# Kernel tuning notes

Hardware: AMD Instinct MI355X
Metric: run time of the kernel (lower is better)

## Reference

```python
import jax, jax.numpy as jnp
import numpy as np

B, S, D = 2, 2048, 2048
H, KV, HD = 32, 8, 64
REP = H // KV  # 4


def setup_inputs() -> dict:
    key = jax.random.key(0)
    ks = jax.random.split(key, 5)
    x = jax.random.normal(ks[0], (B, S, D), jnp.float32)
    # Llama rope frequencies: theta=10000, pairs of adjacent dims
    inv_freq = 1.0 / (10000.0 ** (np.arange(0, HD, 2, dtype=np.float64) / HD))  # [HD/2]
    ang = np.outer(np.arange(S, dtype=np.float64), inv_freq)  # [S, HD/2]
    freqs_cis = jnp.asarray(np.stack([np.cos(ang), np.sin(ang)], axis=-1), jnp.float32)  # [S, HD/2, 2]
    wq = jax.random.normal(ks[1], (H * HD, D), jnp.float32) * 0.02
    wk = jax.random.normal(ks[2], (KV * HD, D), jnp.float32) * 0.02
    wv = jax.random.normal(ks[3], (KV * HD, D), jnp.float32) * 0.02
    wo = jax.random.normal(ks[4], (D, H * HD), jnp.float32) * 0.02
    return {"x": x, "freqs_cis": freqs_cis, "wq": wq, "wk": wk, "wv": wv, "wo": wo}


def _apply_rope(t, cos, sin):
    # t: [B,S,nh,HD]; cos/sin: [S,HD/2]; complex multiply on adjacent pairs
    b, s, nh, hd = t.shape
    t2 = t.reshape(b, s, nh, hd // 2, 2)
    tr, ti = t2[..., 0], t2[..., 1]
    c = cos[None, :, None, :]
    sn = sin[None, :, None, :]
    out = jnp.stack([tr * c - ti * sn, tr * sn + ti * c], axis=-1)
    return out.reshape(b, s, nh, hd)


def reference(x, freqs_cis, wq, wk, wv, wo):
    # QKV projections (torch Linear: y = x @ W.T)
    q = jnp.einsum('bsd,ed->bse', x, wq).reshape(B, S, H, HD)
    k = jnp.einsum('bsd,ed->bse', x, wk).reshape(B, S, KV, HD)
    v = jnp.einsum('bsd,ed->bse', x, wv).reshape(B, S, KV, HD)
    cos, sin = freqs_cis[..., 0], freqs_cis[..., 1]
    q = _apply_rope(q, cos, sin)
    k = _apply_rope(k, cos, sin)
    # GQA without materializing repeated K/V: group query heads by KV head
    qg = q.reshape(B, S, KV, REP, HD)
    scale = 1.0 / jnp.sqrt(jnp.asarray(HD, q.dtype))
    scores = jnp.einsum('bsgrd,btgd->bgrst', qg, k) * scale  # [B,KV,REP,S,S]
    causal = jnp.tril(jnp.ones((S, S), bool))
    scores = jnp.where(causal, scores, -jnp.inf)
    p = jax.nn.softmax(scores, axis=-1)
    o = jnp.einsum('bgrst,btgd->bsgrd', p, v).reshape(B, S, H * HD)
    return jnp.einsum('bse,de->bsd', o, wo)
```

## Files before the change

kernel.cpp:

```cpp
#include <hip/hip_runtime.h>
#include <cstdint>
#include <cstddef>

#define B_ 2
#define S_ 2048
#define D_ 2048
#define H_ 32
#define KV_ 8
#define HD_ 64
#define M_ (B_*S_)
#define EQ_ (H_*HD_)
#define EK_ (KV_*HD_)

typedef unsigned short u16;
typedef __attribute__((ext_vector_type(8))) short s16x8;
typedef __attribute__((ext_vector_type(4))) float f32x4;

#define QSCALE 0.18033688011112042f
#define EXPOFF 15.869645449778564f

#if __has_builtin(__builtin_amdgcn_exp2f)
#define EXP2(x) __builtin_amdgcn_exp2f(x)
#else
#define EXP2(x) __expf((x) * 0.6931471805599453f)
#endif

__device__ __forceinline__ u16 f2bf(float f) {
  unsigned u = __float_as_uint(f);
  u += 0x7fffu + ((u >> 16) & 1u);
  return (u16)(u >> 16);
}
__device__ __forceinline__ unsigned pk2(float a, float b) {
  unsigned ua = __float_as_uint(a) + 0x8000u;
  unsigned ub = __float_as_uint(b) + 0x8000u;
  return __builtin_amdgcn_perm(ub, ua, 0x07060302);
}
__device__ __forceinline__ f32x4 mfma16(s16x8 a, s16x8 b, f32x4 c) {
  return __builtin_amdgcn_mfma_f32_16x16x32_bf16(a, b, c, 0, 0, 0);
}
__device__ __forceinline__ void gl_lds16(const void* g, void* l) {
  __builtin_amdgcn_global_load_lds(
      (const __attribute__((address_space(1))) void*)g,
      (__attribute__((address_space(3))) void*)l, 16, 0, 0);
}

__global__ void cast_all(const float4* __restrict__ x, const float4* __restrict__ wq,
                         const float4* __restrict__ wk, const float4* __restrict__ wv,
                         const float4* __restrict__ wo, ushort4* __restrict__ dst) {
  int i = blockIdx.x * 256 + threadIdx.x;
  const float4* src; int off;
  if (i < 2097152)      { src = x;  off = i; }
  else if (i < 3145728) { src = wq; off = i - 2097152; }
  else if (i < 3407872) { src = wk; off = i - 3145728; }
  else if (i < 3670016) { src = wv; off = i - 3407872; }
  else                  { src = wo; off = i - 3670016; }
  float4 v = src[off];
  ushort4 r;
  r.x = f2bf(v.x); r.y = f2bf(v.y); r.z = f2bf(v.z); r.w = f2bf(v.w);
  dst[i] = r;
}

__global__ __launch_bounds__(256)
void gemm_qkv(const u16* __restrict__ A, const u16* __restrict__ Bw,
              u16* __restrict__ qb, u16* __restrict__ kb, u16* __restrict__ vtb,
              const float* __restrict__ fc) {
  __shared__ __align__(16) u16 As[128 * 64];
  __shared__ __align__(16) u16 Bs[96 * 64];
  const int tid  = threadIdx.x;
  const int lane = tid & 63;
  const int wave = tid >> 6;
  const int m0 = blockIdx.y * 128;
  const int n0 = blockIdx.x * 96;
  const int wm = (wave >> 1) * 64;
  const int wn = (wave & 1) * 48;
  const int l15 = lane & 15;
  const int quad = lane >> 4;

  f32x4 acc[4][3] = {};

  for (int k0 = 0; k0 < D_; k0 += 64) {
    #pragma unroll
    for (int rr = 0; rr < 4; ++rr) {
      int c = tid + rr * 256;
      int row = c >> 3;
      int ksrc = ((c & 7) ^ (row & 7)) * 8;
      gl_lds16(A + (size_t)(m0 + row) * D_ + k0 + ksrc, &As[c * 8]);
    }
    #pragma unroll
    for (int rr = 0; rr < 3; ++rr) {
      int c = tid + rr * 256;
      int row = c >> 3;
      int ksrc = ((c & 7) ^ (row & 7)) * 8;
      gl_lds16(Bw + (size_t)(n0 + row) * D_ + k0 + ksrc, &Bs[c * 8]);
    }
    __syncthreads();

    #pragma unroll
    for (int kc = 0; kc < 2; ++kc) {
      s16x8 af[4], bfr[3];
      #pragma unroll
      for (int mi = 0; mi < 4; ++mi) {
        int row = wm + mi * 16 + l15;
        af[mi]  = *(const s16x8*)&As[row * 64 + (((kc * 4 + quad) ^ (row & 7)) * 8)];
      }
      #pragma unroll
      for (int ni = 0; ni < 3; ++ni) {
        int row = wn + ni * 16 + l15;
        bfr[ni] = *(const s16x8*)&Bs[row * 64 + (((kc * 4 + quad) ^ (row & 7)) * 8)];
      }
      #pragma unroll
      for (int mi = 0; mi < 4; ++mi)
        #pragma unroll
        for (int ni = 0; ni < 3; ++ni)
          acc[mi][ni] = mfma16(af[mi], bfr[ni], acc[mi][ni]);
    }
    __syncthreads();
  }

  const float sg = (l15 & 1) ? 1.f : -1.f;
  #pragma unroll
  for (int mi = 0; mi < 4; ++mi) {
    #pragma unroll
    for (int ni = 0; ni < 3; ++ni) {
      const int col = n0 + wn + ni * 16 + l15;
      if (col < 2560) {
        const bool isQ = (col < 2048);
        u16* dst = isQ ? qb : kb;
        const int ncol0 = isQ ? 0 : 2048;
        const int ndim  = isQ ? EQ_ : EK_;
        const float scale = isQ ? QSCALE : 1.0f;
        const int ip = (col & 63) >> 1;
        #pragma unroll
        for (int r = 0; r < 4; ++r) {
          int row = m0 + wm + mi * 16 + quad * 4 + r;
          const float* fr = fc + (size_t)(row & (S_ - 1)) * 64;
          float c  = fr[ip * 2];
          float sn = fr[ip * 2 + 1];
          float v = acc[mi][ni][r];
          float p = __shfl_xor(v, 1, 64);
          float o = (v * c + sg * (p * sn)) * scale;
          dst[(size_t)row * ndim + col - ncol0] = f2bf(o);
        }
      } else {
        const int vcol = col - 2560;
        uint2 w;
        w.x = pk2(acc[mi][ni][0], acc[mi][ni][1]);
        w.y = pk2(acc[mi][ni][2], acc[mi][ni][3]);
        *(uint2*)(vtb + (size_t)vcol * M_ + m0 + wm + mi * 16 + quad * 4) = w;
      }
    }
  }
}

__global__ __launch_bounds__(256)
void gemm_o(const u16* __restrict__ A, const u16* __restrict__ Bw, float* __restrict__ C,
            int Ndim, int Kdim) {
  __shared__ __align__(16) u16 As[64 * 64];
  __shared__ __align__(16) u16 Bs[128 * 64];
  const int tid  = threadIdx.x;
  const int lane = tid & 63;
  const int wave = tid >> 6;
  const int m0 = blockIdx.y * 64;
  const int n0 = blockIdx.x * 128;
  const int wm = (wave >> 1) * 32;
  const int wn = (wave & 1) * 64;
  const int l15 = lane & 15;
  const int quad = lane >> 4;

  f32x4 acc[2][4] = {};

  for (int k0 = 0; k0 < Kdim; k0 += 64) {
    #pragma unroll
    for (int rr = 0; rr < 2; ++rr) {
      int c = tid + rr * 256;
      int row = c >> 3;
      int ksrc = ((c & 7) ^ (row & 7)) * 8;
      gl_lds16(A + (size_t)(m0 + row) * Kdim + k0 + ksrc, &As[c * 8]);
    }
    #pragma unroll
    for (int rr = 0; rr < 4; ++rr) {
      int c = tid + rr * 256;
      int row = c >> 3;
      int ksrc = ((c & 7) ^ (row & 7)) * 8;
      gl_lds16(Bw + (size_t)(n0 + row) * Kdim + k0 + ksrc, &Bs[c * 8]);
    }
    __syncthreads();

    #pragma unroll
    for (int kc = 0; kc < 2; ++kc) {
      s16x8 af[2], bfr[4];
      #pragma unroll
      for (int mi = 0; mi < 2; ++mi) {
        int row = wm + mi * 16 + l15;
        af[mi]  = *(const s16x8*)&As[row * 64 + (((kc * 4 + quad) ^ (row & 7)) * 8)];
      }
      #pragma unroll
      for (int ni = 0; ni < 4; ++ni) {
        int row = wn + ni * 16 + l15;
        bfr[ni] = *(const s16x8*)&Bs[row * 64 + (((kc * 4 + quad) ^ (row & 7)) * 8)];
      }
      #pragma unroll
      for (int mi = 0; mi < 2; ++mi)
        #pragma unroll
        for (int ni = 0; ni < 4; ++ni)
          acc[mi][ni] = mfma16(af[mi], bfr[ni], acc[mi][ni]);
    }
    __syncthreads();
  }

  #pragma unroll
  for (int mi = 0; mi < 2; ++mi) {
    #pragma unroll
    for (int r = 0; r < 4; ++r) {
      int row = m0 + wm + mi * 16 + quad * 4 + r;
      size_t base = (size_t)row * Ndim + n0 + wn;
      #pragma unroll
      for (int ni = 0; ni < 4; ++ni)
        C[base + ni * 16 + l15] = acc[mi][ni][r];
    }
  }
}

__global__ __launch_bounds__(256, 4)
void flash_attn(const u16* __restrict__ qb, const u16* __restrict__ kb,
                const u16* __restrict__ vtb, u16* __restrict__ ob) {
  const int bx = blockIdx.x;
  const int h  = blockIdx.y;
  const int b  = blockIdx.z;
  const int g  = h >> 2;
  const int tid  = threadIdx.x;
  const int lane = tid & 63;
  const int wave = tid >> 6;
  const int l15  = lane & 15;
  const int quad = lane >> 4;
  const int kq   = quad * 8;

  const int Tlo = bx, Thi = 31 - bx;
  const int n_lo = Tlo + 1, n_hi = Thi + 1;
  const int rL = Tlo * 64 + wave * 16;
  const int rH = Thi * 64 + wave * 16;
  const int rowL = rL + l15;
  const int rowH = rH + l15;

  __shared__ __align__(16) u16 Ks[2][8 * 512];
  __shared__ __align__(16) u16 Vs[8 * 512];
  __shared__ __align__(16) u16 Pl[4][2][16 * 64];

  char* PbL = (char*)&Pl[wave][0][0];
  char* PbH = (char*)&Pl[wave][1][0];
  const int pm = (l15 & 7) << 4;

  const u16* qpL = qb + (size_t)(b * S_ + rL + l15) * EQ_ + h * HD_;
  const u16* qpH = qb + (size_t)(b * S_ + rH + l15) * EQ_ + h * HD_;
  s16x8 qL0 = *(const s16x8*)(qpL + kq);
  s16x8 qL1 = *(const s16x8*)(qpL + 32 + kq);
  s16x8 qH0 = *(const s16x8*)(qpH + kq);
  s16x8 qH1 = *(const s16x8*)(qpH + 32 + kq);

  f32x4 OL[4] = {}, OH[4] = {};
  float sumL = 0.f, sumH = 0.f;

  const int sw = wave & 1;
  const bool doK = (wave < 2);

  const u16* stbase;
  size_t     tstride;
  if (doK) {
    stbase  = kb + (size_t)(b * S_ + lane) * EK_ + g * HD_ + sw * 32;
    tstride = (size_t)64 * EK_;
  } else {
    stbase  = vtb + (size_t)(g * HD_ + lane) * M_ + b * S_ + sw * 32;
    tstride = 64;
  }
  const int ldoff = sw * 4 * 512 + lane * 8;

  if (doK) {
    #pragma unroll
    for (int r = 0; r < 4; ++r)
      gl_lds16(stbase + r * 8, &Ks[0][ldoff + r * 512]);
  }
  __syncthreads();

  for (int kt = 0; kt < n_hi; ++kt) {
    const int t0 = kt * 64;
    const u16* kcur = &Ks[kt & 1][0];

    if (doK) {
      if (kt + 1 < n_hi) {
        const u16* src = stbase + (size_t)(kt + 1) * tstride;
        u16* dst = &Ks[(kt + 1) & 1][ldoff];
        #pragma unroll
        for (int r = 0; r < 4; ++r)
          gl_lds16(src + r * 8, dst + r * 512);
      }
    } else {
      const u16* src = stbase + (size_t)kt * tstride;
      #pragma unroll
      for (int r = 0; r < 4; ++r)
        gl_lds16(src + r * 8, &Vs[ldoff + r * 512]);
    }

    const bool do_lo = (kt < n_lo);
    const bool mH = (kt == n_hi - 1);
    const bool mL = (kt == n_lo - 1);

    #pragma unroll
    for (int ts = 0; ts < 4; ++ts) {
      s16x8 k0 = *(const s16x8*)&kcur[quad * 512 + (ts * 16 + l15) * 8];
      s16x8 k1 = *(const s16x8*)&kcur[(4 + quad) * 512 + (ts * 16 + l15) * 8];
      const int tb = t0 + ts * 16 + quad * 4;
      {
        f32x4 s = {};
        s = mfma16(k0, qH0, s);
        s = mfma16(k1, qH1, s);
        if (mH) {
          #pragma unroll
          for (int r = 0; r < 4; ++r) if (tb + r > rowH) s[r] = -1e30f;
        }
        float p0 = EXP2(s[0] - EXPOFF), p1 = EXP2(s[1] - EXPOFF);
        float p2 = EXP2(s[2] - EXPOFF), p3 = EXP2(s[3] - EXPOFF);
        sumH += (p0 + p1) + (p2 + p3);
        uint2 w; w.x = pk2(p0, p1); w.y = pk2(p2, p3);
        *(uint2*)(PbH + l15 * 128 + ((ts * 32 + quad * 8) ^ pm)) = w;
      }
      if (do_lo) {
        f32x4 s = {};
        s = mfma16(k0, qL0, s);
        s = mfma16(k1, qL1, s);
        if (mL) {
          #pragma unroll
          for (int r = 0; r < 4; ++r) if (tb + r > rowL) s[r] = -1e30f;
        }
        float p0 = EXP2(s[0] - EXPOFF), p1 = EXP2(s[1] - EXPOFF);
        float p2 = EXP2(s[2] - EXPOFF), p3 = EXP2(s[3] - EXPOFF);
        sumL += (p0 + p1) + (p2 + p3);
        uint2 w; w.x = pk2(p0, p1); w.y = pk2(p2, p3);
        *(uint2*)(PbL + l15 * 128 + ((ts * 32 + quad * 8) ^ pm)) = w;
      }
    }

    s16x8 pH0 = *(const s16x8*)(PbH + l15 * 128 + ((quad * 16) ^ pm));
    s16x8 pH1 = *(const s16x8*)(PbH + l15 * 128 + ((64 + quad * 16) ^ pm));
    s16x8 pL0 = {}, pL1 = {};
    if (do_lo) {
      pL0 = *(const s16x8*)(PbL + l15 * 128 + ((quad * 16) ^ pm));
      pL1 = *(const s16x8*)(PbL + l15 * 128 + ((64 + quad * 16) ^ pm));
    }

    __syncthreads();

    #pragma unroll
    for (int df = 0; df < 4; ++df) {
      s16x8 v0 = *(const s16x8*)&Vs[quad * 512 + (df * 16 + l15) * 8];
      s16x8 v1 = *(const s16x8*)&Vs[(4 + quad) * 512 + (df * 16 + l15) * 8];
      OH[df] = mfma16(v1, pH1, mfma16(v0, pH0, OH[df]));
      if (do_lo) OL[df] = mfma16(v1, pL1, mfma16(v0, pL0, OL[df]));
    }

    __syncthreads();
  }

  sumH += __shfl_xor(sumH, 16, 64); sumH += __shfl_xor(sumH, 32, 64);
  sumL += __shfl_xor(sumL, 16, 64); sumL += __shfl_xor(sumL, 32, 64);
  float invH = 1.f / sumH, invL = 1.f / sumL;

  {
    u16* op = ob + (size_t)(b * S_ + rowH) * EQ_ + h * HD_;
    #pragma unroll
    for (int df = 0; df < 4; ++df) {
      uint2 w;
      w.x = pk2(OH[df][0] * invH, OH[df][1] * invH);
      w.y = pk2(OH[df][2] * invH, OH[df][3] * invH);
      *(uint2*)(op + df * 16 + quad * 4) = w;
    }
  }
  {
    u16* op = ob + (size_t)(b * S_ + rowL) * EQ_ + h * HD_;
    #pragma unroll
    for (int df = 0; df < 4; ++df) {
      uint2 w;
      w.x = pk2(OL[df][0] * invL, OL[df][1] * invL);
      w.y = pk2(OL[df][2] * invL, OL[df][3] * invL);
      *(uint2*)(op + df * 16 + quad * 4) = w;
    }
  }
}

extern "C" void kernel_launch(void* const* d_in, const int* in_sizes, int n_in,
                              void* d_out, int out_size, void* d_ws, size_t ws_size,
                              hipStream_t stream) {
  (void)in_sizes; (void)n_in; (void)out_size; (void)ws_size;
  const float* x  = (const float*)d_in[0];
  const float* fc = (const float*)d_in[1];
  const float* wq = (const float*)d_in[2];
  const float* wk = (const float*)d_in[3];
  const float* wv = (const float*)d_in[4];
  const float* wo = (const float*)d_in[5];
  float* out = (float*)d_out;
  char* ws = (char*)d_ws;

  u16* xb  = (u16*)(ws);
  u16* wqb = (u16*)(ws + 16777216);
  u16* wob = (u16*)(ws + 29360128);
  u16* qb  = (u16*)(ws + 37748736);
  u16* kb  = (u16*)(ws + 54525952);
  u16* vtb = (u16*)(ws + 58720256);
  u16* ob  = (u16*)(ws + 62914560);

  cast_all<<<18432, 256, 0, stream>>>((const float4*)x, (const float4*)wq,
                                      (const float4*)wk, (const float4*)wv,
                                      (const float4*)wo, (ushort4*)ws);

  gemm_qkv<<<dim3(32, 32), 256, 0, stream>>>(xb, wqb, qb, kb, vtb, fc);

  flash_attn<<<dim3(16, 32, 2), 256, 0, stream>>>(qb, kb, vtb, ob);

  gemm_o<<<dim3(16, 64), 256, 0, stream>>>(ob, wob, out, D_, EQ_);
}
```

Measured before the change: 301.3 us.

## Double-buffer LDS tiles in QKV and output GEMMs with BK=32 prefetch

Both GEMM kernels now keep two LDS buffers with a K-step of 32 and issue the global-to-LDS copy for the next step before computing on the current one. This leaves one barrier per iteration instead of two and lets global memory latency overlap with MFMA work. The XOR swizzle is reworked for 32-element rows and the per-thread source pointers are precomputed once. The cost is twice as many loop iterations with fewer MFMAs per barrier, and the prefetch depends on the async LDS load completing before the next barrier.

Result: slower. 308.6 us (+2.4%).

```diff
diff --git a/kernel.cpp b/kernel.cpp
--- a/kernel.cpp
+++ b/kernel.cpp
@@ -64,8 +64,8 @@
 void gemm_qkv(const u16* __restrict__ A, const u16* __restrict__ Bw,
               u16* __restrict__ qb, u16* __restrict__ kb, u16* __restrict__ vtb,
               const float* __restrict__ fc) {
-  __shared__ __align__(16) u16 As[128 * 64];
-  __shared__ __align__(16) u16 Bs[96 * 64];
+  __shared__ __align__(16) u16 As[2][128 * 32];
+  __shared__ __align__(16) u16 Bs[2][96 * 32];
   const int tid  = threadIdx.x;
   const int lane = tid & 63;
   const int wave = tid >> 6;
@@ -76,44 +76,53 @@
   const int l15 = lane & 15;
   const int quad = lane >> 4;
 
+  const int ca0 = tid,      ra0 = ca0 >> 2, pa0 = ca0 & 3;
+  const int ca1 = tid + 256, ra1 = ca1 >> 2, pa1 = ca1 & 3;
+  const int cb0 = tid,      rb0 = cb0 >> 2, pb0 = cb0 & 3;
+  const int cb1 = tid + 256, rb1 = cb1 >> 2, pb1 = cb1 & 3;
+  const u16* Ap0 = A + (size_t)(m0 + ra0) * D_ + (pa0 ^ ((ra0 >> 1) & 3)) * 8;
+  const u16* Ap1 = A + (size_t)(m0 + ra1) * D_ + (pa1 ^ ((ra1 >> 1) & 3)) * 8;
+  const u16* Bp0 = Bw + (size_t)(n0 + rb0) * D_ + (pb0 ^ ((rb0 >> 1) & 3)) * 8;
+  const u16* Bp1 = Bw + (size_t)(n0 + rb1) * D_ + (pb1 ^ ((rb1 >> 1) & 3)) * 8;
+  const bool doB1 = (tid < 128);
+
   f32x4 acc[4][3] = {};
 
-  for (int k0 = 0; k0 < D_; k0 += 64) {
-    #pragma unroll
-    for (int rr = 0; rr < 4; ++rr) {
-      int c = tid + rr * 256;
-      int row = c >> 3;
-      int ksrc = ((c & 7) ^ (row & 7)) * 8;
-      gl_lds16(A + (size_t)(m0 + row) * D_ + k0 + ksrc, &As[c * 8]);
-    }
-    #pragma unroll
-    for (int rr = 0; rr < 3; ++rr) {
-      int c = tid + rr * 256;
-      int row = c >> 3;
-      int ksrc = ((c & 7) ^ (row & 7)) * 8;
-      gl_lds16(Bw + (size_t)(n0 + row) * D_ + k0 + ksrc, &Bs[c * 8]);
-    }
-    __syncthreads();
-
-    #pragma unroll
-    for (int kc = 0; kc < 2; ++kc) {
-      s16x8 af[4], bfr[3];
+  gl_lds16(Ap0, &As[0][ca0 * 8]);
+  gl_lds16(Ap1, &As[0][ca1 * 8]);
+  gl_lds16(Bp0, &Bs[0][cb0 * 8]);
+  if (doB1) gl_lds16(Bp1, &Bs[0][cb1 * 8]);
+  __syncthreads();
+
+  for (int ks = 0; ks < 64; ++ks) {
+    if (ks + 1 < 64) {
+      const int nb = (ks + 1) & 1;
+      const int ko = (ks + 1) * 32;
+      gl_lds16(Ap0 + ko, &As[nb][ca0 * 8]);
+      gl_lds16(Ap1 + ko, &As[nb][ca1 * 8]);
+      gl_lds16(Bp0 + ko, &Bs[nb][cb0 * 8]);
+      if (doB1) gl_lds16(Bp1 + ko, &Bs[nb][cb1 * 8]);
+    }
+
+    const u16* as = &As[ks & 1][0];
+    const u16* bs = &Bs[ks & 1][0];
+    s16x8 af[4], bfr[3];
+    #pragma unroll
+    for (int mi = 0; mi < 4; ++mi) {
+      int row = wm + mi * 16 + l15;
+      af[mi] = *(const s16x8*)&as[row * 32 + (quad ^ ((row >> 1) & 3)) * 8];
+    }
+    #pragma unroll
+    for (int ni = 0; ni < 3; ++ni) {
+      int row = wn + ni * 16 + l15;
+      bfr[ni] = *(const s16x8*)&bs[row * 32 + (quad ^ ((row >> 1) & 3)) * 8];
+    }
+    #pragma unroll
+    for (int mi = 0; mi < 4; ++mi)
       #pragma unroll
-      for (int mi = 0; mi < 4; ++mi) {
-        int row = wm + mi * 16 + l15;
-        af[mi]  = *(const s16x8*)&As[row * 64 + (((kc * 4 + quad) ^ (row & 7)) * 8)];
-      }
-      #pragma unroll
-      for (int ni = 0; ni < 3; ++ni) {
-        int row = wn + ni * 16 + l15;
-        bfr[ni] = *(const s16x8*)&Bs[row * 64 + (((kc * 4 + quad) ^ (row & 7)) * 8)];
-      }
-      #pragma unroll
-      for (int mi = 0; mi < 4; ++mi)
-        #pragma unroll
-        for (int ni = 0; ni < 3; ++ni)
-          acc[mi][ni] = mfma16(af[mi], bfr[ni], acc[mi][ni]);
-    }
+      for (int ni = 0; ni < 3; ++ni)
+        acc[mi][ni] = mfma16(af[mi], bfr[ni], acc[mi][ni]);
+
     __syncthreads();
   }
 
@@ -155,8 +164,8 @@
 __global__ __launch_bounds__(256)
 void gemm_o(const u16* __restrict__ A, const u16* __restrict__ Bw, float* __restrict__ C,
             int Ndim, int Kdim) {
-  __shared__ __align__(16) u16 As[64 * 64];
-  __shared__ __align__(16) u16 Bs[128 * 64];
+  __shared__ __align__(16) u16 As[2][64 * 32];
+  __shared__ __align__(16) u16 Bs[2][128 * 32];
   const int tid  = threadIdx.x;
   const int lane = tid & 63;
   const int wave = tid >> 6;
@@ -167,44 +176,50 @@
   const int l15 = lane & 15;
   const int quad = lane >> 4;
 
+  const int ca0 = tid,      ra0 = ca0 >> 2, pa0 = ca0 & 3;
+  const int cb0 = tid,      rb0 = cb0 >> 2, pb0 = cb0 & 3;
+  const int cb1 = tid + 256, rb1 = cb1 >> 2, pb1 = cb1 & 3;
+  const u16* Ap0 = A + (size_t)(m0 + ra0) * Kdim + (pa0 ^ ((ra0 >> 1) & 3)) * 8;
+  const u16* Bp0 = Bw + (size_t)(n0 + rb0) * Kdim + (pb0 ^ ((rb0 >> 1) & 3)) * 8;
+  const u16* Bp1 = Bw + (size_t)(n0 + rb1) * Kdim + (pb1 ^ ((rb1 >> 1) & 3)) * 8;
+
   f32x4 acc[2][4] = {};
 
-  for (int k0 = 0; k0 < Kdim; k0 += 64) {
-    #pragma unroll
-    for (int rr = 0; rr < 2; ++rr) {
-      int c = tid + rr * 256;
-      int row = c >> 3;
-      int ksrc = ((c & 7) ^ (row & 7)) * 8;
-      gl_lds16(A + (size_t)(m0 + row) * Kdim + k0 + ksrc, &As[c * 8]);
-    }
-    #pragma unroll
-    for (int rr = 0; rr < 4; ++rr) {
-      int c = tid + rr * 256;
-      int row = c >> 3;
-      int ksrc = ((c & 7) ^ (row & 7)) * 8;
-      gl_lds16(Bw + (size_t)(n0 + row) * Kdim + k0 + ksrc, &Bs[c * 8]);
-    }
-    __syncthreads();
-
-    #pragma unroll
-    for (int kc = 0; kc < 2; ++kc) {
-      s16x8 af[2], bfr[4];
+  const int nsteps = Kdim >> 5;
+
+  gl_lds16(Ap0, &As[0][ca0 * 8]);
+  gl_lds16(Bp0, &Bs[0][cb0 * 8]);
+  gl_lds16(Bp1, &Bs[0][cb1 * 8]);
+  __syncthreads();
+
+  for (int ks = 0; ks < nsteps; ++ks) {
+    if (ks + 1 < nsteps) {
+      const int nb = (ks + 1) & 1;
+      const int ko = (ks + 1) * 32;
+      gl_lds16(Ap0 + ko, &As[nb][ca0 * 8]);
+      gl_lds16(Bp0 + ko, &Bs[nb][cb0 * 8]);
+      gl_lds16(Bp1 + ko, &Bs[nb][cb1 * 8]);
+    }
+
+    const u16* as = &As[ks & 1][0];
+    const u16* bs = &Bs[ks & 1][0];
+    s16x8 af[2], bfr[4];
+    #pragma unroll
+    for (int mi = 0; mi < 2; ++mi) {
+      int row = wm + mi * 16 + l15;
+      af[mi] = *(const s16x8*)&as[row * 32 + (quad ^ ((row >> 1) & 3)) * 8];
+    }
+    #pragma unroll
+    for (int ni = 0; ni < 4; ++ni) {
+      int row = wn + ni * 16 + l15;
+      bfr[ni] = *(const s16x8*)&bs[row * 32 + (quad ^ ((row >> 1) & 3)) * 8];
+    }
+    #pragma unroll
+    for (int mi = 0; mi < 2; ++mi)
       #pragma unroll
-      for (int mi = 0; mi < 2; ++mi) {
-        int row = wm + mi * 16 + l15;
-        af[mi]  = *(const s16x8*)&As[row * 64 + (((kc * 4 + quad) ^ (row & 7)) * 8)];
-      }
-      #pragma unroll
-      for (int ni = 0; ni < 4; ++ni) {
-        int row = wn + ni * 16 + l15;
-        bfr[ni] = *(const s16x8*)&Bs[row * 64 + (((kc * 4 + quad) ^ (row & 7)) * 8)];
-      }
-      #pragma unroll
-      for (int mi = 0; mi < 2; ++mi)
-        #pragma unroll
-        for (int ni = 0; ni < 4; ++ni)
-          acc[mi][ni] = mfma16(af[mi], bfr[ni], acc[mi][ni]);
-    }
+      for (int ni = 0; ni < 4; ++ni)
+        acc[mi][ni] = mfma16(af[mi], bfr[ni], acc[mi][ni]);
+
     __syncthreads();
   }
 
```
